# Kernel optimization log

Hardware: AMD Instinct MI355X
Metric: run time of the kernel (lower is better)

Reference implementation:

```python
import jax, jax.numpy as jnp
import numpy as np
import math
from itertools import product

N_LEVELS = 16
LOG2_HASHMAP = 19
BASE_RES = 16
N_POINTS = 2 ** 21


def _level_config():
    hashmap_size = round(math.pow(2, LOG2_HASHMAP))
    per_level_scale = math.exp(math.log(2048 * 1 / BASE_RES) / (N_LEVELS - 1))
    offsets, scales, resolutions, hashed = [], [], [], []
    n_params = 0
    for i in range(N_LEVELS):
        scale = math.pow(2.0, i * math.log2(per_level_scale)) * BASE_RES - 1.0
        res = int(math.ceil(scale)) + 1
        p = int(math.ceil(math.pow(res, 3) / 8) * 8)
        p = min(p, hashmap_size)
        hashed.append(math.pow(res, 3) > p)
        offsets.append(n_params)
        scales.append(scale)
        resolutions.append(res)
        n_params += p
    return offsets, scales, resolutions, hashed, n_params, hashmap_size


def setup_inputs() -> dict:
    key = jax.random.key(0)
    k1, k2 = jax.random.split(key)
    _, _, _, _, n_params, _ = _level_config()
    # points in [0, 0.9) to stay inside each dense grid (matches valid NeRF AABB usage)
    x = jax.random.uniform(k1, (N_POINTS, 3), dtype=jnp.float32) * 0.9
    grid = jax.random.uniform(k2, (n_params, 2), dtype=jnp.float32,
                              minval=-1e-4, maxval=1e-4)
    return {"x": x, "grid": grid}


def reference(x, grid):
    offsets, scales, resolutions, hashed, n_params, hashmap_size = _level_config()
    # 8 trilinear corners, z fastest (matches itertools.product order in original)
    corners_np = np.array(list(product([0, 1], repeat=3)), dtype=np.uint32)  # (8,3)
    corners = jnp.asarray(corners_np)
    corner_mask = jnp.asarray(corners_np.astype(bool))
    primes = jnp.array([1, 2654435761, 805459861], dtype=jnp.uint32)
    outs = []
    for lvl in range(N_LEVELS):
        pos = jnp.float32(scales[lvl]) * x + 0.5          # (N,3)
        fl = jnp.floor(pos)
        frac = pos - fl                                    # (N,3)
        base = fl.astype(jnp.uint32)                       # (N,3)
        cg = base[:, None, :] + corners[None, :, :]        # (N,8,3) uint32
        # trilinear weights: prod over dims of frac or 1-frac per corner
        w = jnp.prod(jnp.where(corner_mask[None, :, :],
                               frac[:, None, :], 1.0 - frac[:, None, :]),
                     axis=-1)                              # (N,8)
        if hashed[lvl]:
            h = cg * primes                                # uint32 wraparound mul
            idx = (h[..., 0] ^ h[..., 1] ^ h[..., 2]) % jnp.uint32(hashmap_size)
        else:
            res = resolutions[lvl]
            stride = jnp.array([1, res, res * res], dtype=jnp.uint32)
            idx = jnp.sum(cg * stride, axis=-1)            # (N,8)
        vals = grid[idx + jnp.uint32(offsets[lvl])]        # (N,8,2) gather
        outs.append(jnp.sum(vals * w[..., None], axis=1))  # (N,2)
    # (N, n_levels, 2) -> (N, 32)
    return jnp.stack(outs, axis=1).reshape(x.shape[0], N_LEVELS * 2)
```

## Files before the change

kernel.cpp:

```cpp
#include <hip/hip_runtime.h>
#include <cmath>

#define NLVL 16
#define NDENSE 5
#define TPB 256
#define NP 2

struct LevelCfg { float scale; unsigned offset; unsigned res; };
struct DCfg { LevelCfg lv[NDENSE]; };

__global__ __launch_bounds__(TPB) void khash_kernel(
    const float* __restrict__ x,
    const float2* __restrict__ grid,
    float2* __restrict__ out2,
    float scale, unsigned hm_mask, unsigned slot)
{
  const unsigned P1 = 2654435761u, P2 = 805459861u;
  const unsigned base = blockIdx.x * (TPB * NP) + threadIdx.x;

  unsigned pts[NP], b0v[NP];
  unsigned restv[NP][4];
  float wx[NP][2], wy[NP][2], wz[NP][2];
  float4 q[NP][4];
  float2 oa[NP][4], ob[NP][4];

#pragma unroll
  for (int p = 0; p < NP; ++p) {
    const unsigned pt = base + (unsigned)p * TPB;
    pts[p] = pt;
    const float px = x[pt * 3u + 0u];
    const float py = x[pt * 3u + 1u];
    const float pz = x[pt * 3u + 2u];

    const float p0 = __fadd_rn(__fmul_rn(scale, px), 0.5f);
    const float p1 = __fadd_rn(__fmul_rn(scale, py), 0.5f);
    const float p2 = __fadd_rn(__fmul_rn(scale, pz), 0.5f);
    const float fl0 = floorf(p0), fl1 = floorf(p1), fl2 = floorf(p2);
    const float fr0 = __fsub_rn(p0, fl0);
    const float fr1 = __fsub_rn(p1, fl1);
    const float fr2 = __fsub_rn(p2, fl2);
    const unsigned b0 = (unsigned)fl0, b1 = (unsigned)fl1, b2 = (unsigned)fl2;
    b0v[p] = b0;

    const unsigned hy0 = b1 * P1, hy1 = hy0 + P1;
    const unsigned hz0 = b2 * P2, hz1 = hz0 + P2;
    restv[p][0] = hy0 ^ hz0; restv[p][1] = hy0 ^ hz1;
    restv[p][2] = hy1 ^ hz0; restv[p][3] = hy1 ^ hz1;

    wx[p][0] = __fsub_rn(1.0f, fr0); wx[p][1] = fr0;
    wy[p][0] = __fsub_rn(1.0f, fr1); wy[p][1] = fr1;
    wz[p][0] = __fsub_rn(1.0f, fr2); wz[p][1] = fr2;
  }

#pragma unroll
  for (int p = 0; p < NP; ++p) {
    const unsigned b0 = b0v[p];
    if ((b0 & 1u) == 0u) {
      const float4* __restrict__ g4 = (const float4*)grid;
#pragma unroll
      for (int j = 0; j < 4; ++j) {
        const unsigned i0 = (b0 ^ restv[p][j]) & hm_mask;
        q[p][j] = g4[i0 >> 1];
      }
    }
    if ((b0v[p] & 1u) != 0u) {
#pragma unroll
      for (int j = 0; j < 4; ++j) {
        const unsigned i0 = (b0v[p] ^ restv[p][j]) & hm_mask;
        const unsigned i1 = ((b0v[p] + 1u) ^ restv[p][j]) & hm_mask;
        oa[p][j] = grid[i0];
        ob[p][j] = grid[i1];
      }
    }
  }

#pragma unroll
  for (int p = 0; p < NP; ++p) {
    const unsigned b0 = b0v[p];
    const bool beven = (b0 & 1u) == 0u;
    float ax = 0.0f, ay = 0.0f;
#pragma unroll
    for (int j = 0; j < 4; ++j) {
      const unsigned i0 = (b0 ^ restv[p][j]) & hm_mask;
      const bool odd = (i0 & 1u) != 0u;
      const float2 qlo = make_float2(q[p][j].x, q[p][j].y);
      const float2 qhi = make_float2(q[p][j].z, q[p][j].w);
      const float2 v0 = beven ? (odd ? qhi : qlo) : oa[p][j];
      const float2 v1 = beven ? (odd ? qlo : qhi) : ob[p][j];
      const float w0 = __fmul_rn(__fmul_rn(wx[p][0], wy[p][j >> 1]), wz[p][j & 1]);
      const float w1 = __fmul_rn(__fmul_rn(wx[p][1], wy[p][j >> 1]), wz[p][j & 1]);
      ax = __fmaf_rn(v0.x, w0, ax);  ay = __fmaf_rn(v0.y, w0, ay);
      ax = __fmaf_rn(v1.x, w1, ax);  ay = __fmaf_rn(v1.y, w1, ay);
    }
    const unsigned pt = pts[p];
    out2[(pt >> 4) * 256u + slot * 16u + (pt & 15u)] = make_float2(ax, ay);
  }
}

__global__ __launch_bounds__(TPB) void kfinal_kernel(
    const float* __restrict__ x,
    const float2* __restrict__ grid,
    float2* out2,
    DCfg cfg)
{
  __shared__ float s_x[96];
  __shared__ LevelCfg s_cfg[NDENSE];
  const unsigned tid = threadIdx.x;
  const unsigned lvl = tid & 15u;
  const unsigned lp  = tid >> 4;
  const unsigned chunk0 = blockIdx.x * 2u;
  const unsigned pt0 = chunk0 * 16u;

  float2 staged0 = make_float2(0.0f, 0.0f), staged1 = staged0;
  if (lvl >= NDENSE) {
    staged0 = out2[chunk0 * 256u + (lvl - NDENSE) * 16u + lp];
    staged1 = out2[(chunk0 + 1u) * 256u + (lvl - NDENSE) * 16u + lp];
  }

  if (tid < NDENSE) s_cfg[tid] = cfg.lv[tid];
  if (tid < 96u) s_x[tid] = x[pt0 * 3u + tid];
  __syncthreads();

  float ax[2], ay[2];
  if (lvl < NDENSE) {
    const LevelCfg c = s_cfg[lvl];
    const unsigned r = c.res, r2 = r * r;
    const unsigned doff[4] = { 0u, r2, r, r + r2 };

    unsigned i0[2][4];
    float wxv[2][2], wyv[2][2], wzv[2][2];
#pragma unroll
    for (int p = 0; p < 2; ++p) {
      const unsigned lpp = (unsigned)p * 16u + lp;
      const float px = s_x[lpp * 3u + 0u];
      const float py = s_x[lpp * 3u + 1u];
      const float pz = s_x[lpp * 3u + 2u];
      const float p0 = __fadd_rn(__fmul_rn(c.scale, px), 0.5f);
      const float p1 = __fadd_rn(__fmul_rn(c.scale, py), 0.5f);
      const float p2 = __fadd_rn(__fmul_rn(c.scale, pz), 0.5f);
      const float fl0 = floorf(p0), fl1 = floorf(p1), fl2 = floorf(p2);
      const float fr0 = __fsub_rn(p0, fl0);
      const float fr1 = __fsub_rn(p1, fl1);
      const float fr2 = __fsub_rn(p2, fl2);
      const unsigned b0 = (unsigned)fl0, b1 = (unsigned)fl1, b2 = (unsigned)fl2;
      const unsigned dbase = b0 + b1 * r + b2 * r2 + c.offset;
#pragma unroll
      for (int j = 0; j < 4; ++j) i0[p][j] = dbase + doff[j];
      wxv[p][0] = __fsub_rn(1.0f, fr0); wxv[p][1] = fr0;
      wyv[p][0] = __fsub_rn(1.0f, fr1); wyv[p][1] = fr1;
      wzv[p][0] = __fsub_rn(1.0f, fr2); wzv[p][1] = fr2;
    }

    float q[2][4][4];
#pragma unroll
    for (int p = 0; p < 2; ++p)
#pragma unroll
      for (int j = 0; j < 4; ++j)
        __builtin_memcpy(&q[p][j][0], grid + i0[p][j], 16);

#pragma unroll
    for (int p = 0; p < 2; ++p) {
      float axx = 0.0f, ayy = 0.0f;
#pragma unroll
      for (int j = 0; j < 4; ++j) {
        const float w0 = __fmul_rn(__fmul_rn(wxv[p][0], wyv[p][j >> 1]), wzv[p][j & 1]);
        const float w1 = __fmul_rn(__fmul_rn(wxv[p][1], wyv[p][j >> 1]), wzv[p][j & 1]);
        axx = __fmaf_rn(q[p][j][0], w0, axx);  ayy = __fmaf_rn(q[p][j][1], w0, ayy);
        axx = __fmaf_rn(q[p][j][2], w1, axx);  ayy = __fmaf_rn(q[p][j][3], w1, ayy);
      }
      ax[p] = axx; ay[p] = ayy;
    }
  } else {
    ax[0] = staged0.x; ay[0] = staged0.y;
    ax[1] = staged1.x; ay[1] = staged1.y;
  }

  __syncthreads();
  out2[chunk0 * 256u + tid]        = make_float2(ax[0], ay[0]);
  out2[(chunk0 + 1u) * 256u + tid] = make_float2(ax[1], ay[1]);
}

extern "C" void kernel_launch(void* const* d_in, const int* in_sizes, int n_in,
                              void* d_out, int out_size, void* d_ws, size_t ws_size,
                              hipStream_t stream) {
  const float*  x    = (const float*)d_in[0];
  const float2* grid = (const float2*)d_in[1];
  float2*       out2 = (float2*)d_out;

  const unsigned hashmap_size = 1u << 19;
  const double per_level_scale = exp(log(2048.0 * 1.0 / 16.0) / (NLVL - 1));
  const double b = log2(per_level_scale);
  float  scales[NLVL];
  unsigned offsets[NLVL], ress[NLVL];
  unsigned n_params = 0;
  for (int i = 0; i < NLVL; ++i) {
    const double scale = pow(2.0, (double)i * b) * 16.0 - 1.0;
    const int res = (int)ceil(scale) + 1;
    const double res3 = pow((double)res, 3.0);
    unsigned p = (unsigned)(ceil(res3 / 8.0) * 8.0);
    if (p > hashmap_size) p = hashmap_size;
    offsets[i] = n_params;
    scales[i]  = (float)scale;
    ress[i]    = (unsigned)res;
    n_params += p;
  }

  const unsigned n_points = (unsigned)(in_sizes[0] / 3);

  const unsigned nblk_h = n_points / (TPB * NP);
  for (int L = NDENSE; L < NLVL; ++L) {
    khash_kernel<<<nblk_h, TPB, 0, stream>>>(
        x, grid + offsets[L], out2, scales[L], hashmap_size - 1u,
        (unsigned)(L - NDENSE));
  }

  DCfg cfg;
  for (int i = 0; i < NDENSE; ++i) {
    cfg.lv[i].scale  = scales[i];
    cfg.lv[i].offset = offsets[i];
    cfg.lv[i].res    = ress[i];
  }
  kfinal_kernel<<<n_points / 32u, TPB, 0, stream>>>(x, grid, out2, cfg);
}
```

Measured before the change: 766.8 us.

## Spread dense-level trilinear gathers across all lanes with shuffle reduction

The final kernel used to compute the five dense levels on only 5 of every 16 lanes, while the other 11 lanes only copied staged hash results. Now each lane handles one (level, y/z corner pair) for levels 0-3, and lanes 0-3 also take level 4. Partial sums are reduced with xor shuffles and passed through shared memory before the coalesced output write. This balances the gather work across lanes at the cost of extra shuffles, shared-memory traffic and recomputing the position for each corner pair.

```diff
diff --git a/kernel.cpp b/kernel.cpp
--- a/kernel.cpp
+++ b/kernel.cpp
@@ -97,7 +97,7 @@
   }
 }
 
-__global__ __launch_bounds__(TPB) void kfinal_kernel(
+__global__ __launch_bounds__(TPB) void kasm_kernel(
     const float* __restrict__ x,
     const float2* __restrict__ grid,
     float2* out2,
@@ -105,79 +105,103 @@
 {
   __shared__ float s_x[96];
   __shared__ LevelCfg s_cfg[NDENSE];
+  __shared__ float s_fx[32][NDENSE];
+  __shared__ float s_fy[32][NDENSE];
   const unsigned tid = threadIdx.x;
-  const unsigned lvl = tid & 15u;
+  const unsigned sl  = tid & 15u;
   const unsigned lp  = tid >> 4;
+  const unsigned jA  = tid & 3u;
+  const unsigned lvlA = sl >> 2;
   const unsigned chunk0 = blockIdx.x * 2u;
   const unsigned pt0 = chunk0 * 16u;
-
-  float2 staged0 = make_float2(0.0f, 0.0f), staged1 = staged0;
-  if (lvl >= NDENSE) {
-    staged0 = out2[chunk0 * 256u + (lvl - NDENSE) * 16u + lp];
-    staged1 = out2[(chunk0 + 1u) * 256u + (lvl - NDENSE) * 16u + lp];
-  }
 
   if (tid < NDENSE) s_cfg[tid] = cfg.lv[tid];
   if (tid < 96u) s_x[tid] = x[pt0 * 3u + tid];
   __syncthreads();
 
-  float ax[2], ay[2];
-  if (lvl < NDENSE) {
+  auto dense_pair = [&](unsigned pp, unsigned lvl, unsigned j,
+                        unsigned &i0, float &w0, float &w1) {
     const LevelCfg c = s_cfg[lvl];
+    const float px = s_x[pp * 3u + 0u];
+    const float py = s_x[pp * 3u + 1u];
+    const float pz = s_x[pp * 3u + 2u];
+    const float p0 = __fadd_rn(__fmul_rn(c.scale, px), 0.5f);
+    const float p1 = __fadd_rn(__fmul_rn(c.scale, py), 0.5f);
+    const float p2 = __fadd_rn(__fmul_rn(c.scale, pz), 0.5f);
+    const float fl0 = floorf(p0), fl1 = floorf(p1), fl2 = floorf(p2);
+    const float fr0 = __fsub_rn(p0, fl0);
+    const float fr1 = __fsub_rn(p1, fl1);
+    const float fr2 = __fsub_rn(p2, fl2);
+    const unsigned b0 = (unsigned)fl0, b1 = (unsigned)fl1, b2 = (unsigned)fl2;
     const unsigned r = c.res, r2 = r * r;
-    const unsigned doff[4] = { 0u, r2, r, r + r2 };
-
-    unsigned i0[2][4];
-    float wxv[2][2], wyv[2][2], wzv[2][2];
-#pragma unroll
-    for (int p = 0; p < 2; ++p) {
-      const unsigned lpp = (unsigned)p * 16u + lp;
-      const float px = s_x[lpp * 3u + 0u];
-      const float py = s_x[lpp * 3u + 1u];
-      const float pz = s_x[lpp * 3u + 2u];
-      const float p0 = __fadd_rn(__fmul_rn(c.scale, px), 0.5f);
-      const float p1 = __fadd_rn(__fmul_rn(c.scale, py), 0.5f);
-      const float p2 = __fadd_rn(__fmul_rn(c.scale, pz), 0.5f);
-      const float fl0 = floorf(p0), fl1 = floorf(p1), fl2 = floorf(p2);
-      const float fr0 = __fsub_rn(p0, fl0);
-      const float fr1 = __fsub_rn(p1, fl1);
-      const float fr2 = __fsub_rn(p2, fl2);
-      const unsigned b0 = (unsigned)fl0, b1 = (unsigned)fl1, b2 = (unsigned)fl2;
-      const unsigned dbase = b0 + b1 * r + b2 * r2 + c.offset;
-#pragma unroll
-      for (int j = 0; j < 4; ++j) i0[p][j] = dbase + doff[j];
-      wxv[p][0] = __fsub_rn(1.0f, fr0); wxv[p][1] = fr0;
-      wyv[p][0] = __fsub_rn(1.0f, fr1); wyv[p][1] = fr1;
-      wzv[p][0] = __fsub_rn(1.0f, fr2); wzv[p][1] = fr2;
-    }
-
-    float q[2][4][4];
+    const unsigned by = j >> 1, bz = j & 1u;
+    i0 = b0 + b1 * r + b2 * r2 + c.offset + (by ? r : 0u) + (bz ? r2 : 0u);
+    const float wyf = by ? fr1 : __fsub_rn(1.0f, fr1);
+    const float wzf = bz ? fr2 : __fsub_rn(1.0f, fr2);
+    const float wyz = __fmul_rn(wyf, wzf);
+    w0 = __fmul_rn(__fsub_rn(1.0f, fr0), wyz);
+    w1 = __fmul_rn(fr0, wyz);
+  };
+
+  const bool hasB = (sl < 4u);
+  unsigned iA[2], iB[2];
+  float w0A[2], w1A[2], w0B[2], w1B[2];
+#pragma unroll
+  for (int p = 0; p < 2; ++p) {
+    const unsigned pp = (unsigned)p * 16u + lp;
+    dense_pair(pp, lvlA, jA, iA[p], w0A[p], w1A[p]);
+    if (hasB) dense_pair(pp, NDENSE - 1, sl, iB[p], w0B[p], w1B[p]);
+  }
+
+  float qA[2][4], qB[2][4];
+#pragma unroll
+  for (int p = 0; p < 2; ++p)
+    __builtin_memcpy(&qA[p][0], grid + iA[p], 16);
+  if (hasB) {
 #pragma unroll
     for (int p = 0; p < 2; ++p)
-#pragma unroll
-      for (int j = 0; j < 4; ++j)
-        __builtin_memcpy(&q[p][j][0], grid + i0[p][j], 16);
-
-#pragma unroll
-    for (int p = 0; p < 2; ++p) {
-      float axx = 0.0f, ayy = 0.0f;
-#pragma unroll
-      for (int j = 0; j < 4; ++j) {
-        const float w0 = __fmul_rn(__fmul_rn(wxv[p][0], wyv[p][j >> 1]), wzv[p][j & 1]);
-        const float w1 = __fmul_rn(__fmul_rn(wxv[p][1], wyv[p][j >> 1]), wzv[p][j & 1]);
-        axx = __fmaf_rn(q[p][j][0], w0, axx);  ayy = __fmaf_rn(q[p][j][1], w0, ayy);
-        axx = __fmaf_rn(q[p][j][2], w1, axx);  ayy = __fmaf_rn(q[p][j][3], w1, ayy);
-      }
-      ax[p] = axx; ay[p] = ayy;
-    }
-  } else {
-    ax[0] = staged0.x; ay[0] = staged0.y;
-    ax[1] = staged1.x; ay[1] = staged1.y;
+      __builtin_memcpy(&qB[p][0], grid + iB[p], 16);
+  }
+
+  float2 staged[2];
+  staged[0] = make_float2(0.0f, 0.0f); staged[1] = staged[0];
+  if (sl >= NDENSE) {
+#pragma unroll
+    for (int p = 0; p < 2; ++p)
+      staged[p] = out2[(chunk0 + (unsigned)p) * 256u + (sl - NDENSE) * 16u + lp];
+  }
+
+#pragma unroll
+  for (int p = 0; p < 2; ++p) {
+    const unsigned pp = (unsigned)p * 16u + lp;
+    float ax = __fmaf_rn(qA[p][2], w1A[p], __fmul_rn(qA[p][0], w0A[p]));
+    float ay = __fmaf_rn(qA[p][3], w1A[p], __fmul_rn(qA[p][1], w0A[p]));
+    ax = __fadd_rn(ax, __shfl_xor(ax, 1));
+    ay = __fadd_rn(ay, __shfl_xor(ay, 1));
+    ax = __fadd_rn(ax, __shfl_xor(ax, 2));
+    ay = __fadd_rn(ay, __shfl_xor(ay, 2));
+    if (jA == 0u) { s_fx[pp][lvlA] = ax; s_fy[pp][lvlA] = ay; }
+    float bx = 0.0f, by = 0.0f;
+    if (hasB) {
+      bx = __fmaf_rn(qB[p][2], w1B[p], __fmul_rn(qB[p][0], w0B[p]));
+      by = __fmaf_rn(qB[p][3], w1B[p], __fmul_rn(qB[p][1], w0B[p]));
+    }
+    bx = __fadd_rn(bx, __shfl_xor(bx, 1));
+    by = __fadd_rn(by, __shfl_xor(by, 1));
+    bx = __fadd_rn(bx, __shfl_xor(bx, 2));
+    by = __fadd_rn(by, __shfl_xor(by, 2));
+    if (sl == 0u) { s_fx[pp][NDENSE - 1] = bx; s_fy[pp][NDENSE - 1] = by; }
   }
 
   __syncthreads();
-  out2[chunk0 * 256u + tid]        = make_float2(ax[0], ay[0]);
-  out2[(chunk0 + 1u) * 256u + tid] = make_float2(ax[1], ay[1]);
+#pragma unroll
+  for (int p = 0; p < 2; ++p) {
+    const unsigned pp = (unsigned)p * 16u + lp;
+    float2 v;
+    if (sl < NDENSE) v = make_float2(s_fx[pp][sl], s_fy[pp][sl]);
+    else             v = staged[p];
+    out2[(chunk0 + (unsigned)p) * 256u + tid] = v;
+  }
 }
 
 extern "C" void kernel_launch(void* const* d_in, const int* in_sizes, int n_in,
@@ -220,5 +244,5 @@
     cfg.lv[i].offset = offsets[i];
     cfg.lv[i].res    = ress[i];
   }
-  kfinal_kernel<<<n_points / 32u, TPB, 0, stream>>>(x, grid, out2, cfg);
+  kasm_kernel<<<n_points / 32u, TPB, 0, stream>>>(x, grid, out2, cfg);
 }
```

Result: no change. 782.1 us (+2.0%).

## Use nontemporal stores/loads and process four chunks per block with double-buffered gathers

Applied to the files above, without the earlier changes.

Hash-level kernels now write their outputs with nontemporal stores, and the final dense kernel reads those staged values with nontemporal loads. The final kernel handles four 16-point chunks per block instead of two. It precomputes the trilinear weights and double-buffers the grid gathers so loads for point p+2 are issued while point p is being accumulated. The goal is to cut cache pollution from the large output stream and hide gather latency, at the cost of more registers and fewer blocks.

```diff
diff --git a/kernel.cpp b/kernel.cpp
--- a/kernel.cpp
+++ b/kernel.cpp
@@ -5,9 +5,22 @@
 #define NDENSE 5
 #define TPB 256
 #define NP 2
+#define PC 4
 
 struct LevelCfg { float scale; unsigned offset; unsigned res; };
 struct DCfg { LevelCfg lv[NDENSE]; };
+
+static __device__ inline void nt_store_f2(float2* p, float2 v) {
+  unsigned long long u;
+  __builtin_memcpy(&u, &v, 8);
+  __builtin_nontemporal_store(u, (unsigned long long*)p);
+}
+static __device__ inline float2 nt_load_f2(const float2* p) {
+  unsigned long long u = __builtin_nontemporal_load((const unsigned long long*)p);
+  float2 v;
+  __builtin_memcpy(&v, &u, 8);
+  return v;
+}
 
 __global__ __launch_bounds__(TPB) void khash_kernel(
     const float* __restrict__ x,
@@ -93,7 +106,8 @@
       ax = __fmaf_rn(v1.x, w1, ax);  ay = __fmaf_rn(v1.y, w1, ay);
     }
     const unsigned pt = pts[p];
-    out2[(pt >> 4) * 256u + slot * 16u + (pt & 15u)] = make_float2(ax, ay);
+    nt_store_f2(&out2[(pt >> 4) * 256u + slot * 16u + (pt & 15u)],
+                make_float2(ax, ay));
   }
 }
 
@@ -103,34 +117,38 @@
     float2* out2,
     DCfg cfg)
 {
-  __shared__ float s_x[96];
+  __shared__ float s_x[48 * PC];
   __shared__ LevelCfg s_cfg[NDENSE];
   const unsigned tid = threadIdx.x;
   const unsigned lvl = tid & 15u;
   const unsigned lp  = tid >> 4;
-  const unsigned chunk0 = blockIdx.x * 2u;
+  const unsigned chunk0 = blockIdx.x * PC;
   const unsigned pt0 = chunk0 * 16u;
 
-  float2 staged0 = make_float2(0.0f, 0.0f), staged1 = staged0;
+  float2 staged[PC];
+#pragma unroll
+  for (int p = 0; p < PC; ++p) staged[p] = make_float2(0.0f, 0.0f);
   if (lvl >= NDENSE) {
-    staged0 = out2[chunk0 * 256u + (lvl - NDENSE) * 16u + lp];
-    staged1 = out2[(chunk0 + 1u) * 256u + (lvl - NDENSE) * 16u + lp];
+#pragma unroll
+    for (int p = 0; p < PC; ++p)
+      staged[p] = nt_load_f2(
+          &out2[(chunk0 + (unsigned)p) * 256u + (lvl - NDENSE) * 16u + lp]);
   }
 
   if (tid < NDENSE) s_cfg[tid] = cfg.lv[tid];
-  if (tid < 96u) s_x[tid] = x[pt0 * 3u + tid];
+  if (tid < 48u * PC) s_x[tid] = x[pt0 * 3u + tid];
   __syncthreads();
 
-  float ax[2], ay[2];
+  float ax[PC], ay[PC];
   if (lvl < NDENSE) {
     const LevelCfg c = s_cfg[lvl];
     const unsigned r = c.res, r2 = r * r;
     const unsigned doff[4] = { 0u, r2, r, r + r2 };
 
-    unsigned i0[2][4];
-    float wxv[2][2], wyv[2][2], wzv[2][2];
-#pragma unroll
-    for (int p = 0; p < 2; ++p) {
+    unsigned i0[PC][4];
+    float w0[PC][4], w1[PC][4];
+#pragma unroll
+    for (int p = 0; p < PC; ++p) {
       const unsigned lpp = (unsigned)p * 16u + lp;
       const float px = s_x[lpp * 3u + 0u];
       const float py = s_x[lpp * 3u + 1u];
@@ -144,40 +162,52 @@
       const float fr2 = __fsub_rn(p2, fl2);
       const unsigned b0 = (unsigned)fl0, b1 = (unsigned)fl1, b2 = (unsigned)fl2;
       const unsigned dbase = b0 + b1 * r + b2 * r2 + c.offset;
-#pragma unroll
-      for (int j = 0; j < 4; ++j) i0[p][j] = dbase + doff[j];
-      wxv[p][0] = __fsub_rn(1.0f, fr0); wxv[p][1] = fr0;
-      wyv[p][0] = __fsub_rn(1.0f, fr1); wyv[p][1] = fr1;
-      wzv[p][0] = __fsub_rn(1.0f, fr2); wzv[p][1] = fr2;
+      const float wyv[2] = { __fsub_rn(1.0f, fr1), fr1 };
+      const float wzv[2] = { __fsub_rn(1.0f, fr2), fr2 };
+      const float wx0 = __fsub_rn(1.0f, fr0);
+#pragma unroll
+      for (int j = 0; j < 4; ++j) {
+        i0[p][j] = dbase + doff[j];
+        const float wyz = __fmul_rn(wyv[j >> 1], wzv[j & 1]);
+        w0[p][j] = __fmul_rn(wx0, wyz);
+        w1[p][j] = __fmul_rn(fr0, wyz);
+      }
     }
 
     float q[2][4][4];
 #pragma unroll
-    for (int p = 0; p < 2; ++p)
-#pragma unroll
-      for (int j = 0; j < 4; ++j)
-        __builtin_memcpy(&q[p][j][0], grid + i0[p][j], 16);
-
-#pragma unroll
-    for (int p = 0; p < 2; ++p) {
+    for (int j = 0; j < 4; ++j) __builtin_memcpy(&q[0][j][0], grid + i0[0][j], 16);
+#pragma unroll
+    for (int j = 0; j < 4; ++j) __builtin_memcpy(&q[1][j][0], grid + i0[1][j], 16);
+
+#pragma unroll
+    for (int p = 0; p < PC; ++p) {
+      const int buf = p & 1;
       float axx = 0.0f, ayy = 0.0f;
 #pragma unroll
       for (int j = 0; j < 4; ++j) {
-        const float w0 = __fmul_rn(__fmul_rn(wxv[p][0], wyv[p][j >> 1]), wzv[p][j & 1]);
-        const float w1 = __fmul_rn(__fmul_rn(wxv[p][1], wyv[p][j >> 1]), wzv[p][j & 1]);
-        axx = __fmaf_rn(q[p][j][0], w0, axx);  ayy = __fmaf_rn(q[p][j][1], w0, ayy);
-        axx = __fmaf_rn(q[p][j][2], w1, axx);  ayy = __fmaf_rn(q[p][j][3], w1, ayy);
+        axx = __fmaf_rn(q[buf][j][0], w0[p][j], axx);
+        ayy = __fmaf_rn(q[buf][j][1], w0[p][j], ayy);
+        axx = __fmaf_rn(q[buf][j][2], w1[p][j], axx);
+        ayy = __fmaf_rn(q[buf][j][3], w1[p][j], ayy);
       }
       ax[p] = axx; ay[p] = ayy;
+      if (p + 2 < PC) {
+#pragma unroll
+        for (int j = 0; j < 4; ++j)
+          __builtin_memcpy(&q[buf][j][0], grid + i0[p + 2][j], 16);
+      }
     }
   } else {
-    ax[0] = staged0.x; ay[0] = staged0.y;
-    ax[1] = staged1.x; ay[1] = staged1.y;
+#pragma unroll
+    for (int p = 0; p < PC; ++p) { ax[p] = staged[p].x; ay[p] = staged[p].y; }
   }
 
   __syncthreads();
-  out2[chunk0 * 256u + tid]        = make_float2(ax[0], ay[0]);
-  out2[(chunk0 + 1u) * 256u + tid] = make_float2(ax[1], ay[1]);
+#pragma unroll
+  for (int p = 0; p < PC; ++p)
+    nt_store_f2(&out2[(chunk0 + (unsigned)p) * 256u + tid],
+                make_float2(ax[p], ay[p]));
 }
 
 extern "C" void kernel_launch(void* const* d_in, const int* in_sizes, int n_in,
@@ -220,5 +250,5 @@
     cfg.lv[i].offset = offsets[i];
     cfg.lv[i].res    = ress[i];
   }
-  kfinal_kernel<<<n_points / 32u, TPB, 0, stream>>>(x, grid, out2, cfg);
-}
+  kfinal_kernel<<<n_points / (16u * PC), TPB, 0, stream>>>(x, grid, out2, cfg);
+}
```

Measured after the change: 758.0 us. About the same (-1.1%).
